# Performance work log

Hardware: AMD Instinct MI355X
Metric: run time of the kernel (lower is better)

Reference implementation:

```python
import jax, jax.numpy as jnp
import numpy as np

EMB_DIM = 1024
NUM_HEADS = 16
HEAD_DIM = EMB_DIM // NUM_HEADS
B, S_Q, S_KV = 4, 2048, 2048


def setup_inputs() -> dict:
    key = jax.random.key(0)
    ks = jax.random.split(key, 12)
    s = EMB_DIM ** -0.5  # torch Linear default init scale (approx, uniform-like)
    inp = {
        "q": jax.random.normal(ks[0], (B, S_Q, EMB_DIM), jnp.float32),
        "k": jax.random.normal(ks[1], (B, S_KV, EMB_DIM), jnp.float32),
        "v": jax.random.normal(ks[2], (B, S_KV, EMB_DIM), jnp.float32),
        "mask": jax.random.randint(ks[3], (B, S_KV), 0, 2, jnp.int32),
        "Wq": jax.random.normal(ks[4], (EMB_DIM, EMB_DIM), jnp.float32) * s,
        "bq": jnp.zeros((EMB_DIM,), jnp.float32),
        "Wk": jax.random.normal(ks[5], (EMB_DIM, EMB_DIM), jnp.float32) * s,
        "bk": jnp.zeros((EMB_DIM,), jnp.float32),
        "Wv": jax.random.normal(ks[6], (EMB_DIM, EMB_DIM), jnp.float32) * s,
        "bv": jnp.zeros((EMB_DIM,), jnp.float32),
        "Wo": jax.random.normal(ks[7], (EMB_DIM, EMB_DIM), jnp.float32) * s,
        "bo": jnp.zeros((EMB_DIM,), jnp.float32),
    }
    return inp


def reference(q, k, v, mask, Wq, bq, Wk, bk, Wv, bv, Wo, bo):
    Bsz, Sq, E = q.shape
    Skv = k.shape[1]
    H, D = NUM_HEADS, HEAD_DIM
    scale = D ** -0.5

    # projections (torch Linear: x @ W.T + b)
    qh = (q @ Wq.T + bq).reshape(Bsz, Sq, H, D).transpose(0, 2, 1, 3)   # [B,H,Sq,D]
    kh = (k @ Wk.T + bk).reshape(Bsz, Skv, H, D).transpose(0, 2, 1, 3)  # [B,H,Skv,D]
    vh = (v @ Wv.T + bv).reshape(Bsz, Skv, H, D).transpose(0, 2, 1, 3)  # [B,H,Skv,D]

    attn = jnp.einsum("bhqd,bhkd->bhqk", qh, kh) * scale  # [B,H,Sq,Skv]

    valid = mask != 0                                      # [B,Skv]
    all_invalid = ~jnp.any(valid, axis=-1, keepdims=True)  # [B,1]
    safe = valid | all_invalid                             # reopened rows
    attn = jnp.where(safe[:, None, None, :], attn, -jnp.inf)

    attn = jax.nn.softmax(attn, axis=-1)
    attn = jnp.where(all_invalid.reshape(Bsz, 1, 1, 1), 0.0, attn)

    out = jnp.einsum("bhqk,bhkd->bhqd", attn, vh)          # [B,H,Sq,D]
    out = out.transpose(0, 2, 1, 3).reshape(Bsz, Sq, E)
    return out @ Wo.T + bo
```

## Files before the change

kernel.cpp:

```cpp
#include <hip/hip_runtime.h>
#include <hip/hip_bf16.h>

typedef short bh8 __attribute__((ext_vector_type(8)));
typedef float f32x4 __attribute__((ext_vector_type(4)));
typedef float f32x16 __attribute__((ext_vector_type(16)));
typedef float f2 __attribute__((ext_vector_type(2)));
typedef unsigned int uint4v __attribute__((ext_vector_type(4)));

#define GLOBAL_P(p) ((const __attribute__((address_space(1))) void*)(p))
#define LDS_P(p)    ((__attribute__((address_space(3))) void*)(p))

__device__ inline bh8 pack8(const float4& a, const float4& b) {
    union { bh8 v; __hip_bfloat16 h[8]; } u;
    u.h[0] = __float2bfloat16(a.x); u.h[1] = __float2bfloat16(a.y);
    u.h[2] = __float2bfloat16(a.z); u.h[3] = __float2bfloat16(a.w);
    u.h[4] = __float2bfloat16(b.x); u.h[5] = __float2bfloat16(b.y);
    u.h[6] = __float2bfloat16(b.z); u.h[7] = __float2bfloat16(b.w);
    return u.v;
}

__global__ __launch_bounds__(256) void cvt3(
    const float* __restrict__ a, const float* __restrict__ b, const float* __restrict__ c,
    __hip_bfloat16* __restrict__ oa, __hip_bfloat16* __restrict__ ob, __hip_bfloat16* __restrict__ oc)
{
    size_t i = ((size_t)blockIdx.x * 256 + threadIdx.x) * 8;
    float4 x0 = *(const float4*)(a + i), x1 = *(const float4*)(a + i + 4);
    *(bh8*)(oa + i) = pack8(x0, x1);
    float4 y0 = *(const float4*)(b + i), y1 = *(const float4*)(b + i + 4);
    *(bh8*)(ob + i) = pack8(y0, y1);
    float4 z0 = *(const float4*)(c + i), z1 = *(const float4*)(c + i + 4);
    *(bh8*)(oc + i) = pack8(z0, z1);
}

__global__ __launch_bounds__(256) void cvtW(
    const float* __restrict__ a, const float* __restrict__ b,
    const float* __restrict__ c, const float* __restrict__ d,
    __hip_bfloat16* __restrict__ o)
{
    int seg = blockIdx.x >> 9;
    const float* src = (seg == 0) ? a : (seg == 1) ? b : (seg == 2) ? c : d;
    size_t i = ((size_t)(blockIdx.x & 511) * 256 + threadIdx.x) * 8;
    float4 x0 = *(const float4*)(src + i), x1 = *(const float4*)(src + i + 4);
    *(bh8*)(o + (size_t)seg * 1048576 + i) = pack8(x0, x1);
}

__global__ __launch_bounds__(256) void maskScan(
    const int* __restrict__ mask, int* __restrict__ idx, int* __restrict__ nv)
{
    __shared__ int ts[256];
    const int b = blockIdx.x, tid = threadIdx.x;
    int f[8], cnt = 0;
#pragma unroll
    for (int j = 0; j < 8; ++j) {
        f[j] = (mask[b * 2048 + tid * 8 + j] != 0) ? 1 : 0;
        cnt += f[j];
    }
    ts[tid] = cnt;
    __syncthreads();
    for (int off = 1; off < 256; off <<= 1) {
        int v = (tid >= off) ? ts[tid - off] : 0;
        __syncthreads();
        ts[tid] += v;
        __syncthreads();
    }
    int base = ts[tid] - cnt;
#pragma unroll
    for (int j = 0; j < 8; ++j)
        if (f[j]) idx[b * 2048 + base++] = tid * 8 + j;
    if (tid == 255) nv[b] = ts[255];
}

__global__ __launch_bounds__(256) void gatherKV(
    const __hip_bfloat16* __restrict__ Kw, const __hip_bfloat16* __restrict__ Vw,
    const int* __restrict__ idx, const int* __restrict__ nv,
    __hip_bfloat16* __restrict__ Kc, __hip_bfloat16* __restrict__ Vc)
{
    const int b = blockIdx.x >> 5, j = blockIdx.x & 31;
    const int n = nv[b], npad = (n + 63) & ~63;
    const int r = j * 64 + (threadIdx.x >> 2);
    if (r >= npad) return;
    const int c0 = (threadIdx.x & 3) * 256;
    __hip_bfloat16* dk = Kc + ((size_t)b * 2048 + r) * 1024 + c0;
    __hip_bfloat16* dv = Vc + ((size_t)b * 2048 + r) * 1024 + c0;
    if (r < n) {
        const int s = idx[b * 2048 + r];
        const __hip_bfloat16* sk = Kw + ((size_t)b * 2048 + s) * 1024 + c0;
        const __hip_bfloat16* sv = Vw + ((size_t)b * 2048 + s) * 1024 + c0;
#pragma unroll
        for (int i = 0; i < 32; ++i) {
            ((bh8*)dk)[i] = ((const bh8*)sk)[i];
            ((bh8*)dv)[i] = ((const bh8*)sv)[i];
        }
    } else {
        bh8 z = {};
#pragma unroll
        for (int i = 0; i < 32; ++i) { ((bh8*)dk)[i] = z; ((bh8*)dv)[i] = z; }
    }
}

template <typename TC>
__global__ __launch_bounds__(256) void gemm_bt(
    const __hip_bfloat16* __restrict__ A, const __hip_bfloat16* __restrict__ W,
    const float* __restrict__ bias, TC* __restrict__ C,
    int M, int N, int Ksz, float oscale)
{
    __shared__ __hip_bfloat16 As[128 * 64];
    __shared__ __hip_bfloat16 Bs[128 * 64];
    const int tid = threadIdx.x;
    const int l = tid & 63, w = tid >> 6;
    const int g4 = l >> 4, rl = l & 15;
    const int nb = N >> 7;
    const int bm = blockIdx.x / nb, bn = blockIdx.x % nb;
    const long m0 = (long)bm * 128, n0 = (long)bn * 128;

    const __hip_bfloat16* ag[4];
    const __hip_bfloat16* wg[4];
    int ldsbase[4];
#pragma unroll
    for (int i = 0; i < 4; ++i) {
        int c = i * 256 + tid;
        int row = c >> 3, c8 = c & 7;
        ag[i] = A + (m0 + row) * Ksz + c8 * 8;
        wg[i] = W + (n0 + row) * Ksz + c8 * 8;
        ldsbase[i] = (i * 256 + w * 64) * 8;
    }

    const int wr = w >> 1, wc = w & 1;
    f32x4 acc[4][4];
#pragma unroll
    for (int i = 0; i < 4; ++i)
#pragma unroll
        for (int j = 0; j < 4; ++j) acc[i][j] = f32x4{0.f, 0.f, 0.f, 0.f};

    const int nk = Ksz >> 6;
    for (int t = 0; t < nk; ++t) {
        __syncthreads();
#pragma unroll
        for (int i = 0; i < 4; ++i) {
            __builtin_amdgcn_global_load_lds(GLOBAL_P(ag[i]), LDS_P((__hip_bfloat16*)As + ldsbase[i]), 16, 0, 0);
            __builtin_amdgcn_global_load_lds(GLOBAL_P(wg[i]), LDS_P((__hip_bfloat16*)Bs + ldsbase[i]), 16, 0, 0);
            ag[i] += 64; wg[i] += 64;
        }
        __syncthreads();
#pragma unroll
        for (int kc = 0; kc < 2; ++kc) {
            bh8 af[4], bf[4];
#pragma unroll
            for (int mt = 0; mt < 4; ++mt) {
                int row = wr * 64 + mt * 16 + rl;
                af[mt] = *(const bh8*)(As + row * 64 + 8 * g4 + 32 * kc);
            }
#pragma unroll
            for (int nt = 0; nt < 4; ++nt) {
                int row = wc * 64 + nt * 16 + rl;
                bf[nt] = *(const bh8*)(Bs + row * 64 + 8 * g4 + 32 * kc);
            }
#pragma unroll
            for (int mt = 0; mt < 4; ++mt)
#pragma unroll
                for (int nt = 0; nt < 4; ++nt)
                    acc[mt][nt] = __builtin_amdgcn_mfma_f32_16x16x32_bf16(af[mt], bf[nt], acc[mt][nt], 0, 0, 0);
        }
    }

    float bv[4];
#pragma unroll
    for (int nt = 0; nt < 4; ++nt)
        bv[nt] = bias[n0 + wc * 64 + nt * 16 + rl];
#pragma unroll
    for (int mt = 0; mt < 4; ++mt) {
#pragma unroll
        for (int r = 0; r < 4; ++r) {
            long row = m0 + wr * 64 + mt * 16 + g4 * 4 + r;
            TC* cp = C + row * N + n0 + wc * 64 + rl;
#pragma unroll
            for (int nt = 0; nt < 4; ++nt) {
                float x = (acc[mt][nt][r] + bv[nt]) * oscale;
                if constexpr (__is_same(TC, float)) cp[nt * 16] = x;
                else cp[nt * 16] = __float2bfloat16(x);
            }
        }
    }
}

#define THRL 11.0f

__global__ __launch_bounds__(256, 2) void attn_kernel(
    const __hip_bfloat16* __restrict__ Qm, const __hip_bfloat16* __restrict__ Km,
    const __hip_bfloat16* __restrict__ Vm, const int* __restrict__ nvp,
    __hip_bfloat16* __restrict__ Om)
{
    __shared__ __hip_bfloat16 Kt[2][64 * 64];
    __shared__ __hip_bfloat16 Vt[2][64 * 64];
    __shared__ float biasS[2048];
    const int tid = threadIdx.x;
    const int w = tid >> 6, l = tid & 63;
    const int G = l >> 5, c = l & 31;
    const int id = blockIdx.x;
    const int xcd = id & 7, slot = id >> 3;
    const int bh = xcd * 8 + (slot >> 4);
    const int qb = slot & 15;
    const int b = bh >> 4, h = bh & 15;
    const int q0 = qb * 128 + w * 32;

    const int n = nvp[b];
    const int nt = (n + 63) >> 6;

#pragma unroll
    for (int i = 0; i < 8; ++i) {
        int idx = i * 256 + tid;
        biasS[idx] = (idx < n) ? 0.f : -1e30f;
    }

    const __hip_bfloat16* qp = Qm + (size_t)(b * 2048 + q0 + c) * 1024 + h * 64 + 8 * G;
    bh8 qf[4];
#pragma unroll
    for (int kc = 0; kc < 4; ++kc) qf[kc] = *(const bh8*)(qp + 16 * kc);

    const int l38 = l >> 3, lc8 = l & 7;
    const __hip_bfloat16* kg0 = Km + (size_t)(b * 2048 + 16 * w + l38) * 1024 + h * 64 + 8 * ((lc8 ^ l38 ^ (2 * w)) & 7);
    const __hip_bfloat16* kg1 = Km + (size_t)(b * 2048 + 16 * w + 8 + l38) * 1024 + h * 64 + 8 * ((lc8 ^ l38 ^ (2 * w + 1)) & 7);
    const int kbase_e = w * 1024;

    const int vpi = tid >> 3, vd0 = (tid & 7) * 8;
    const __hip_bfloat16* vbase = Vm + (size_t)(b * 2048 + 2 * vpi) * 1024 + h * 64 + vd0;

    bh8 va0, va1;
    auto loadV = [&](int tt) {
        const __hip_bfloat16* vp = vbase + (size_t)tt * 64 * 1024;
        va0 = *(const bh8*)vp;
        va1 = *(const bh8*)(vp + 1024);
    };
    auto stageV = [&](int buf) {
        __hip_bfloat16* dst = &Vt[buf][0];
#pragma unroll
        for (int j = 0; j < 8; ++j) {
            int d = vd0 + j;
            int swz = ((d & 7) ^ (d >> 3)) << 3;
            unsigned lo = (unsigned short)((const short*)&va0)[j];
            unsigned hi = (unsigned short)((const short*)&va1)[j];
            *(unsigned*)&dst[(d * 64 + 2 * vpi) ^ swz] = lo | (hi << 16);
        }
    };
    auto stageK = [&](int buf, int tt) {
        const size_t off = (size_t)tt * 64 * 1024;
        __builtin_amdgcn_global_load_lds(GLOBAL_P(kg0 + off), LDS_P(&Kt[buf][0] + kbase_e), 16, 0, 0);
        __builtin_amdgcn_global_load_lds(GLOBAL_P(kg1 + off), LDS_P(&Kt[buf][0] + kbase_e + 512), 16, 0, 0);
    };

    stageK(0, 0);
    loadV(0);
    stageV(0);
    loadV(nt > 1 ? 1 : 0);
    __syncthreads();

    f32x16 o0 = {0.f}, o1 = {0.f};
    float m_run = -1e29f, l_run = 0.f;

    for (int t = 0; t < nt; ++t) {
        const int buf = t & 1;
        if (t < nt - 1) {
            stageK(buf ^ 1, t + 1);
            stageV(buf ^ 1);
            loadV(t + 2 < nt ? t + 2 : nt - 1);
        }
        __builtin_amdgcn_sched_barrier(0);

        const __hip_bfloat16* kbuf = &Kt[buf][0];
        const int kx0 = ((c & 7) ^ (c >> 3)) << 3;
        const int kx1 = kx0 ^ 32;
        f32x16 s0 = {0.f}, s1 = {0.f};
        __builtin_amdgcn_s_setprio(1);
#pragma unroll
        for (int kc = 0; kc < 4; ++kc) {
            bh8 kf = *(const bh8*)(kbuf + c * 64 + ((16 * kc + 8 * G) ^ kx0));
            s0 = __builtin_amdgcn_mfma_f32_32x32x16_bf16(kf, qf[kc], s0, 0, 0, 0);
        }
#pragma unroll
        for (int kc = 0; kc < 4; ++kc) {
            bh8 kf = *(const bh8*)(kbuf + (c + 32) * 64 + ((16 * kc + 8 * G) ^ kx1));
            s1 = __builtin_amdgcn_mfma_f32_32x32x16_bf16(kf, qf[kc], s1, 0, 0, 0);
        }
        __builtin_amdgcn_s_setprio(0);

        f2 mx2 = {-1e30f, -1e30f};
#pragma unroll
        for (int ct = 0; ct < 2; ++ct) {
            f2* sp = (f2*)(ct ? &s1 : &s0);
#pragma unroll
            for (int i2 = 0; i2 < 8; ++i2) {
                const int i = i2 * 2;
                f2 bb = *(const f2*)&biasS[t * 64 + ct * 32 + (i >> 2) * 8 + 4 * G + (i & 3)];
                f2 sv = sp[i2] + bb;
                sp[i2] = sv;
                mx2 = __builtin_elementwise_max(mx2, sv);
            }
        }
        float mxl = fmaxf(mx2[0], mx2[1]);

        if (__all(mxl - m_run <= THRL)) {
            f2 ls2 = {0.f, 0.f};
            f2 m2 = {m_run, m_run};
#pragma unroll
            for (int ct = 0; ct < 2; ++ct) {
                f2* sp = (f2*)(ct ? &s1 : &s0);
#pragma unroll
                for (int i2 = 0; i2 < 8; ++i2) {
                    f2 e = sp[i2] - m2;
                    f2 p;
                    p[0] = __builtin_amdgcn_exp2f(e[0]);
                    p[1] = __builtin_amdgcn_exp2f(e[1]);
                    sp[i2] = p; ls2 += p;
                }
            }
            l_run += ls2[0] + ls2[1];
        } else {
            float mxf = fmaxf(mxl, __shfl_xor(mxl, 32));
            const float m_new = fmaxf(m_run, mxf);
            const float fac = __builtin_amdgcn_exp2f(m_run - m_new);
            f2 ls2 = {0.f, 0.f};
            f2 m2 = {m_new, m_new};
#pragma unroll
            for (int ct = 0; ct < 2; ++ct) {
                f2* sp = (f2*)(ct ? &s1 : &s0);
#pragma unroll
                for (int i2 = 0; i2 < 8; ++i2) {
                    f2 e = sp[i2] - m2;
                    f2 p;
                    p[0] = __builtin_amdgcn_exp2f(e[0]);
                    p[1] = __builtin_amdgcn_exp2f(e[1]);
                    sp[i2] = p; ls2 += p;
                }
            }
            l_run = l_run * fac + (ls2[0] + ls2[1]);
            m_run = m_new;
            f2 fc = {fac, fac};
            f2* o0p = (f2*)&o0; f2* o1p = (f2*)&o1;
#pragma unroll
            for (int i2 = 0; i2 < 8; ++i2) { o0p[i2] *= fc; o1p[i2] *= fc; }
        }

        const __hip_bfloat16* vbuf = &Vt[buf][0];
        const int swz0 = ((c & 7) ^ (c >> 3)) << 3;
        const int swz1 = ((c & 7) ^ ((c + 32) >> 3)) << 3;
#pragma unroll
        for (int sl = 0; sl < 4; ++sl) {
            const f32x16& ps = (sl < 2) ? s0 : s1;
            const int R0 = 8 * (sl & 1);
            unsigned a0, a1, b0, b1;
            asm("v_cvt_pk_bf16_f32 %0, %1, %2" : "=v"(a0) : "v"(ps[R0 + 0]), "v"(ps[R0 + 1]));
            asm("v_cvt_pk_bf16_f32 %0, %1, %2" : "=v"(a1) : "v"(ps[R0 + 2]), "v"(ps[R0 + 3]));
            asm("v_cvt_pk_bf16_f32 %0, %1, %2" : "=v"(b0) : "v"(ps[R0 + 4]), "v"(ps[R0 + 5]));
            asm("v_cvt_pk_bf16_f32 %0, %1, %2" : "=v"(b1) : "v"(ps[R0 + 6]), "v"(ps[R0 + 7]));
            asm("v_permlane32_swap_b32 %0, %1" : "+v"(a0), "+v"(b0));
            asm("v_permlane32_swap_b32 %0, %1" : "+v"(a1), "+v"(b1));
            uint4v pu = {a0, a1, b0, b1};
            bh8 pf = __builtin_bit_cast(bh8, pu);
            const int kvb = 16 * sl + 8 * G;
            bh8 vf0 = *(const bh8*)(vbuf + c * 64 + (kvb ^ swz0));
            bh8 vf1 = *(const bh8*)(vbuf + (c + 32) * 64 + (kvb ^ swz1));
            __builtin_amdgcn_s_setprio(1);
            o0 = __builtin_amdgcn_mfma_f32_32x32x16_bf16(vf0, pf, o0, 0, 0, 0);
            o1 = __builtin_amdgcn_mfma_f32_32x32x16_bf16(vf1, pf, o1, 0, 0, 0);
            __builtin_amdgcn_s_setprio(0);
        }

        __syncthreads();
    }

    float l_tot = l_run + __shfl_xor(l_run, 32);
    float inv = (l_tot > 0.f) ? 1.f / l_tot : 0.f;
    __hip_bfloat16* op = Om + (size_t)(b * 2048 + q0 + c) * 1024 + h * 64 + 4 * G;
#pragma unroll
    for (int dt = 0; dt < 2; ++dt) {
#pragma unroll
        for (int rb = 0; rb < 4; ++rb) {
            union { ushort4 u; __hip_bfloat16 hv[4]; } cv;
#pragma unroll
            for (int j = 0; j < 4; ++j) {
                float x = (dt ? o1[rb * 4 + j] : o0[rb * 4 + j]) * inv;
                cv.hv[j] = __float2bfloat16(x);
            }
            *(ushort4*)(op + dt * 32 + rb * 8) = cv.u;
        }
    }
}

extern "C" void kernel_launch(void* const* d_in, const int* in_sizes, int n_in,
                              void* d_out, int out_size, void* d_ws, size_t ws_size,
                              hipStream_t stream) {
    const float* q  = (const float*)d_in[0];
    const float* k  = (const float*)d_in[1];
    const float* v  = (const float*)d_in[2];
    const int*   mk = (const int*)d_in[3];
    const float* Wq = (const float*)d_in[4];
    const float* bq = (const float*)d_in[5];
    const float* Wk = (const float*)d_in[6];
    const float* bk = (const float*)d_in[7];
    const float* Wv = (const float*)d_in[8];
    const float* bv = (const float*)d_in[9];
    const float* Wo = (const float*)d_in[10];
    const float* bo = (const float*)d_in[11];
    float* out = (float*)d_out;

    const float CSC = 0.18033688011112042f;
    const size_t MN = (size_t)8192 * 1024;
    const size_t WN = (size_t)1024 * 1024;
    __hip_bfloat16* R0 = (__hip_bfloat16*)d_ws;
    __hip_bfloat16* R1 = R0 + MN;
    __hip_bfloat16* R2 = R1 + MN;
    __hip_bfloat16* R3 = R2 + MN;
    __hip_bfloat16* Wb = R3 + MN;
    int* idxp = (int*)(Wb + 4 * WN);
    int* nvp  = idxp + 4 * 2048;
    __hip_bfloat16* Vc = (__hip_bfloat16*)((char*)idxp + 33024);

    cvt3<<<4096, 256, 0, stream>>>(q, k, v, R0, R1, R2);
    cvtW<<<2048, 256, 0, stream>>>(Wq, Wk, Wv, Wo, Wb);
    maskScan<<<4, 256, 0, stream>>>(mk, idxp, nvp);
    gemm_bt<__hip_bfloat16><<<512, 256, 0, stream>>>(R0, Wb,          bq, R3, 8192, 1024, 1024, CSC);
    gemm_bt<__hip_bfloat16><<<512, 256, 0, stream>>>(R1, Wb + WN,     bk, R0, 8192, 1024, 1024, 1.0f);
    gemm_bt<__hip_bfloat16><<<512, 256, 0, stream>>>(R2, Wb + 2 * WN, bv, R1, 8192, 1024, 1024, 1.0f);
    gatherKV<<<128, 256, 0, stream>>>(R0, R1, idxp, nvp, R2, Vc);
    attn_kernel<<<1024, 256, 0, stream>>>(R3, R2, Vc, nvp, R0);
    gemm_bt<float><<<512, 256, 0, stream>>>(R0, Wb + 3 * WN, bo, out, 8192, 1024, 1024, 1.0f);
}
```

Measured before the change: 237.8 us.

## Gather valid K/V tokens before projection and skip padded GEMM tiles

Valid-token compaction now happens on the raw fp32 K/V inputs, and the bf16 conversion is fused into the gather, before the projections run. Earlier it happened after projection. The K and V projection GEMMs then return early for 128-row tiles beyond each batch's padded valid count. This removes roughly the masked fraction of K/V projection FLOPs, the K/V conversion traffic for masked tokens, and a separate bf16 gather pass. Padding is raised to 128 so it lines up with the GEMM tile. The cost is a gather that reads scattered fp32 rows.

```diff
diff --git a/kernel.cpp b/kernel.cpp
--- a/kernel.cpp
+++ b/kernel.cpp
@@ -19,17 +19,12 @@
     return u.v;
 }
 
-__global__ __launch_bounds__(256) void cvt3(
-    const float* __restrict__ a, const float* __restrict__ b, const float* __restrict__ c,
-    __hip_bfloat16* __restrict__ oa, __hip_bfloat16* __restrict__ ob, __hip_bfloat16* __restrict__ oc)
+__global__ __launch_bounds__(256) void cvt1(
+    const float* __restrict__ a, __hip_bfloat16* __restrict__ oa)
 {
     size_t i = ((size_t)blockIdx.x * 256 + threadIdx.x) * 8;
     float4 x0 = *(const float4*)(a + i), x1 = *(const float4*)(a + i + 4);
     *(bh8*)(oa + i) = pack8(x0, x1);
-    float4 y0 = *(const float4*)(b + i), y1 = *(const float4*)(b + i + 4);
-    *(bh8*)(ob + i) = pack8(y0, y1);
-    float4 z0 = *(const float4*)(c + i), z1 = *(const float4*)(c + i + 4);
-    *(bh8*)(oc + i) = pack8(z0, z1);
 }
 
 __global__ __launch_bounds__(256) void cvtW(
@@ -70,39 +65,39 @@
     if (tid == 255) nv[b] = ts[255];
 }
 
-__global__ __launch_bounds__(256) void gatherKV(
-    const __hip_bfloat16* __restrict__ Kw, const __hip_bfloat16* __restrict__ Vw,
+__global__ __launch_bounds__(256) void gatherTok(
+    const float* __restrict__ kf, const float* __restrict__ vf,
     const int* __restrict__ idx, const int* __restrict__ nv,
-    __hip_bfloat16* __restrict__ Kc, __hip_bfloat16* __restrict__ Vc)
-{
-    const int b = blockIdx.x >> 5, j = blockIdx.x & 31;
-    const int n = nv[b], npad = (n + 63) & ~63;
-    const int r = j * 64 + (threadIdx.x >> 2);
-    if (r >= npad) return;
+    __hip_bfloat16* __restrict__ kc, __hip_bfloat16* __restrict__ vc)
+{
+    const int b = blockIdx.x >> 5, rb = blockIdx.x & 31;
+    const int n = nv[b], np = (n + 127) & ~127;
+    const int r = rb * 64 + (threadIdx.x >> 2);
+    if (r >= np) return;
     const int c0 = (threadIdx.x & 3) * 256;
-    __hip_bfloat16* dk = Kc + ((size_t)b * 2048 + r) * 1024 + c0;
-    __hip_bfloat16* dv = Vc + ((size_t)b * 2048 + r) * 1024 + c0;
+    bh8* dk = (bh8*)(kc + ((size_t)b * 2048 + r) * 1024 + c0);
+    bh8* dv = (bh8*)(vc + ((size_t)b * 2048 + r) * 1024 + c0);
     if (r < n) {
         const int s = idx[b * 2048 + r];
-        const __hip_bfloat16* sk = Kw + ((size_t)b * 2048 + s) * 1024 + c0;
-        const __hip_bfloat16* sv = Vw + ((size_t)b * 2048 + s) * 1024 + c0;
+        const float4* sk = (const float4*)(kf + ((size_t)b * 2048 + s) * 1024 + c0);
+        const float4* sv = (const float4*)(vf + ((size_t)b * 2048 + s) * 1024 + c0);
 #pragma unroll
         for (int i = 0; i < 32; ++i) {
-            ((bh8*)dk)[i] = ((const bh8*)sk)[i];
-            ((bh8*)dv)[i] = ((const bh8*)sv)[i];
+            dk[i] = pack8(sk[2 * i], sk[2 * i + 1]);
+            dv[i] = pack8(sv[2 * i], sv[2 * i + 1]);
         }
     } else {
         bh8 z = {};
 #pragma unroll
-        for (int i = 0; i < 32; ++i) { ((bh8*)dk)[i] = z; ((bh8*)dv)[i] = z; }
-    }
-}
-
-template <typename TC>
+        for (int i = 0; i < 32; ++i) { dk[i] = z; dv[i] = z; }
+    }
+}
+
+template <typename TC, bool COMPACT>
 __global__ __launch_bounds__(256) void gemm_bt(
     const __hip_bfloat16* __restrict__ A, const __hip_bfloat16* __restrict__ W,
     const float* __restrict__ bias, TC* __restrict__ C,
-    int M, int N, int Ksz, float oscale)
+    int M, int N, int Ksz, float oscale, const int* __restrict__ nvp)
 {
     __shared__ __hip_bfloat16 As[128 * 64];
     __shared__ __hip_bfloat16 Bs[128 * 64];
@@ -111,6 +106,10 @@
     const int g4 = l >> 4, rl = l & 15;
     const int nb = N >> 7;
     const int bm = blockIdx.x / nb, bn = blockIdx.x % nb;
+    if constexpr (COMPACT) {
+        const int np = (nvp[bm >> 4] + 127) & ~127;
+        if ((bm & 15) * 128 >= np) return;
+    }
     const long m0 = (long)bm * 128, n0 = (long)bn * 128;
 
     const __hip_bfloat16* ag[4];
@@ -413,15 +412,14 @@
     __hip_bfloat16* Wb = R3 + MN;
     int* idxp = (int*)(Wb + 4 * WN);
     int* nvp  = idxp + 4 * 2048;
-    __hip_bfloat16* Vc = (__hip_bfloat16*)((char*)idxp + 33024);
-
-    cvt3<<<4096, 256, 0, stream>>>(q, k, v, R0, R1, R2);
+
+    cvt1<<<4096, 256, 0, stream>>>(q, R0);
     cvtW<<<2048, 256, 0, stream>>>(Wq, Wk, Wv, Wo, Wb);
     maskScan<<<4, 256, 0, stream>>>(mk, idxp, nvp);
-    gemm_bt<__hip_bfloat16><<<512, 256, 0, stream>>>(R0, Wb,          bq, R3, 8192, 1024, 1024, CSC);
-    gemm_bt<__hip_bfloat16><<<512, 256, 0, stream>>>(R1, Wb + WN,     bk, R0, 8192, 1024, 1024, 1.0f);
-    gemm_bt<__hip_bfloat16><<<512, 256, 0, stream>>>(R2, Wb + 2 * WN, bv, R1, 8192, 1024, 1024, 1.0f);
-    gatherKV<<<128, 256, 0, stream>>>(R0, R1, idxp, nvp, R2, Vc);
-    attn_kernel<<<1024, 256, 0, stream>>>(R3, R2, Vc, nvp, R0);
-    gemm_bt<float><<<512, 256, 0, stream>>>(R0, Wb + 3 * WN, bo, out, 8192, 1024, 1024, 1.0f);
-}
+    gatherTok<<<128, 256, 0, stream>>>(k, v, idxp, nvp, R1, R2);
+    gemm_bt<__hip_bfloat16, false><<<512, 256, 0, stream>>>(R0, Wb,          bq, R3, 8192, 1024, 1024, CSC,  nullptr);
+    gemm_bt<__hip_bfloat16, true ><<<512, 256, 0, stream>>>(R1, Wb + WN,     bk, R0, 8192, 1024, 1024, 1.0f, nvp);
+    gemm_bt<__hip_bfloat16, true ><<<512, 256, 0, stream>>>(R2, Wb + 2 * WN, bv, R1, 8192, 1024, 1024, 1.0f, nvp);
+    attn_kernel<<<1024, 256, 0, stream>>>(R3, R0, R1, nvp, R2);
+    gemm_bt<float, false><<<512, 256, 0, stream>>>(R2, Wb + 3 * WN, bo, out, 8192, 1024, 1024, 1.0f, nullptr);
+}
```

Result: faster. 230.5 us (-3.1%).
